# Kernel optimization log

Hardware: AMD Instinct MI355X
Metric: run time of the kernel (lower is better)

Reference implementation:

```python
import jax, jax.numpy as jnp
import numpy as np

WINDOW = 3
SEQ_LEN = 41
FEATURE = 128
FILTER_NUM = 128
PAD = WINDOW // 2


def setup_inputs() -> dict:
    key = jax.random.key(0)
    k1, k2 = jax.random.split(key)
    B = 4096
    inputs = jax.random.normal(k1, (B, SEQ_LEN, FEATURE), dtype=jnp.float32)
    # per-position Linear weights: 41 independent [window*feature -> filter_num] layers
    fan_in = WINDOW * FEATURE
    W = jax.random.normal(k2, (SEQ_LEN, fan_in, FILTER_NUM), dtype=jnp.float32) / np.sqrt(fan_in)
    b = jnp.zeros((SEQ_LEN, FILTER_NUM), dtype=jnp.float32)
    return {"inputs": inputs, "W": W, "b": b}


def reference(inputs, W, b):
    # inputs: [B, S, F]; pad sequence dim by PAD zeros on each side
    xpad = jnp.pad(inputs, ((0, 0), (PAD, PAD), (0, 0)))  # [B, S+2*PAD, F]
    # gather windows: idx[s, w] = s + w -> [B, S, WINDOW, F]
    idx = jnp.arange(SEQ_LEN)[:, None] + jnp.arange(WINDOW)[None, :]
    xw = xpad[:, idx, :]
    B = inputs.shape[0]
    xw = xw.reshape(B, SEQ_LEN, WINDOW * FEATURE)  # [B, S, W*F]
    # per-position linear (locally-connected): one batched GEMM over positions
    out = jnp.einsum('bsd,sdf->bsf', xw, W) + b[None, :, :]
    # ReLU; Dropout(0.5) is identity in eval mode
    return jax.nn.relu(out)
```

## Files before the change

kernel.cpp:

```cpp
#include <hip/hip_runtime.h>

#define SEQ 41
#define FEAT 128
#define KDIM 384
#define ROWLEN (SEQ * FEAT)
#define BM 128

typedef float floatx4 __attribute__((ext_vector_type(4)));
typedef __bf16 bf16x8 __attribute__((ext_vector_type(8)));
typedef unsigned short ushortx8 __attribute__((ext_vector_type(8)));

__device__ __forceinline__ unsigned short f2bf(float f) {
    unsigned int u = __builtin_bit_cast(unsigned int, f);
    return (unsigned short)((u + 0x7fffu + ((u >> 16) & 1u)) >> 16);
}

__device__ __forceinline__ bf16x8 pack8(floatx4 lo, floatx4 hi) {
    bf16x8 r;
#pragma unroll
    for (int j = 0; j < 4; j++) { r[j] = (__bf16)lo[j]; r[4 + j] = (__bf16)hi[j]; }
    return r;
}

__global__ __launch_bounds__(256) void wt2_kernel(const float* __restrict__ W,
                                                  unsigned short* __restrict__ Wt2) {
    int t = blockIdx.x * 256 + threadIdx.x;
    int s = t / 6144, g = t % 6144;
    int lane = g & 63, nt = (g >> 6) & 7, ks = (g >> 9) & 1, slab = g >> 10;
    int n  = nt * 16 + (lane & 15);
    int k0 = slab * 64 + ks * 32 + (lane >> 4) * 8;
    const float* Ws = W + (size_t)s * KDIM * FEAT;
    ushortx8 v;
#pragma unroll
    for (int j = 0; j < 8; j++) v[j] = f2bf(Ws[(size_t)(k0 + j) * FEAT + n]);
    *reinterpret_cast<ushortx8*>(Wt2 + (size_t)t * 8) = v;
}

template <int USE_WT>
__global__ __launch_bounds__(256, 3) void gemm_kernel(const float* __restrict__ X,
                                                      const void* __restrict__ Wsrc,
                                                      const float* __restrict__ bias,
                                                      float* __restrict__ out) {
    const int tid  = threadIdx.x;
    const int lane = tid & 63;
    const int wv   = tid >> 6;
    const int s    = blockIdx.y;
    const int m0   = blockIdx.x * BM + wv * 32;

    const int klo = (s == 0) ? 2 : 0;
    const int khi = (s == SEQ - 1) ? 4 : 6;
    const int nst = (khi - klo) * 2;

    const int colq = lane & 15, quad = lane >> 4;

    const int koff = (s - 1) * FEAT + klo * 64 + quad * 8;
    const float* aptr0 = X + (size_t)(m0 + colq) * ROWLEN + koff;
    const float* aptr1 = aptr0 + (size_t)16 * ROWLEN;

    const unsigned short* Wt2 = (const unsigned short*)Wsrc;
    const float* Wf = (const float*)Wsrc;
    const unsigned short* bptr = Wt2 + ((size_t)s * 6 + klo) * 8192 + lane * 8;

    floatx4 acc[2][8];
#pragma unroll
    for (int mi = 0; mi < 2; mi++)
#pragma unroll
        for (int ni = 0; ni < 8; ni++) acc[mi][ni] = (floatx4){0.f, 0.f, 0.f, 0.f};

    floatx4 aL0[2], aH0[2], aL1[2], aH1[2];

    auto loadA = [&](floatx4 (&L)[2], floatx4 (&H)[2], int ksi) {
        const float* p0 = aptr0 + ksi * 32;
        const float* p1 = aptr1 + ksi * 32;
        L[0] = *reinterpret_cast<const floatx4*>(p0);
        H[0] = *reinterpret_cast<const floatx4*>(p0 + 4);
        L[1] = *reinterpret_cast<const floatx4*>(p1);
        H[1] = *reinterpret_cast<const floatx4*>(p1 + 4);
    };

    auto step = [&](floatx4 (&L)[2], floatx4 (&H)[2], int ksi) {
        bf16x8 bfr[8];
        if (USE_WT) {
            const unsigned short* bp = bptr + (size_t)ksi * 4096;
#pragma unroll
            for (int ni = 0; ni < 8; ni++)
                bfr[ni] = *reinterpret_cast<const bf16x8*>(bp + ni * 512);
        } else {
            int kk = klo * 64 + ksi * 32 + quad * 8;
#pragma unroll
            for (int ni = 0; ni < 8; ni++) {
                ushortx8 v;
#pragma unroll
                for (int j = 0; j < 8; j++)
                    v[j] = f2bf(Wf[((size_t)s * KDIM + kk + j) * FEAT + ni * 16 + colq]);
                bfr[ni] = __builtin_bit_cast(bf16x8, v);
            }
        }
        bf16x8 af0 = pack8(L[0], H[0]);
        bf16x8 af1 = pack8(L[1], H[1]);
        __builtin_amdgcn_s_setprio(1);
#pragma unroll
        for (int ni = 0; ni < 8; ni++) {
            acc[0][ni] = __builtin_amdgcn_mfma_f32_16x16x32_bf16(af0, bfr[ni], acc[0][ni], 0, 0, 0);
            acc[1][ni] = __builtin_amdgcn_mfma_f32_16x16x32_bf16(af1, bfr[ni], acc[1][ni], 0, 0, 0);
        }
        __builtin_amdgcn_s_setprio(0);
    };

    loadA(aL0, aH0, 0);
    for (int ksi = 0; ksi < nst; ksi += 2) {
        loadA(aL1, aH1, ksi + 1);
        step(aL0, aH0, ksi);
        if (ksi + 2 < nst) loadA(aL0, aH0, ksi + 2);
        step(aL1, aH1, ksi + 1);
    }

#pragma unroll
    for (int ni = 0; ni < 8; ni++) {
        int n = ni * 16 + colq;
        float bv = bias[s * FEAT + n];
#pragma unroll
        for (int mi = 0; mi < 2; mi++) {
            size_t base = ((size_t)(m0 + mi * 16 + quad * 4) * SEQ + s) * FEAT + n;
#pragma unroll
            for (int r = 0; r < 4; r++) {
                float v = acc[mi][ni][r] + bv;
                v = v > 0.f ? v : 0.f;
                out[base + (size_t)r * (SEQ * FEAT)] = v;
            }
        }
    }
}

extern "C" void kernel_launch(void* const* d_in, const int* in_sizes, int n_in,
                              void* d_out, int out_size, void* d_ws, size_t ws_size,
                              hipStream_t stream) {
    const float* X    = (const float*)d_in[0];
    const float* W    = (const float*)d_in[1];
    const float* bias = (const float*)d_in[2];
    float* out = (float*)d_out;

    const int B = in_sizes[0] / ROWLEN;
    dim3 grid(B / BM, SEQ);

    const size_t wt_bytes = (size_t)SEQ * 6 * 8192 * sizeof(unsigned short);
    if (ws_size >= wt_bytes) {
        unsigned short* Wt2 = (unsigned short*)d_ws;
        wt2_kernel<<<(SEQ * 6144) / 256, 256, 0, stream>>>(W, Wt2);
        gemm_kernel<1><<<grid, 256, 0, stream>>>(X, (const void*)Wt2, bias, out);
    } else {
        gemm_kernel<0><<<grid, 256, 0, stream>>>(X, (const void*)W, bias, out);
    }
}
```

Before: 202.3 us.

## Stage per-position weights in LDS via async DMA with larger 512-thread tiles

The GEMM block grows to 256 rows and 8 waves. The whole per-position bf16 weight slab (up to 96KB) is loaded once into shared memory with global_load_lds, so waves no longer each read B fragments from global/L2. The A loads are prefetched four steps deep in registers to hide latency. In exchange there is a large LDS footprint that limits occupancy, a full-slab barrier before any compute, and more register pressure from the four A buffers.

```diff
diff --git a/kernel.cpp b/kernel.cpp
--- a/kernel.cpp
+++ b/kernel.cpp
@@ -4,7 +4,7 @@
 #define FEAT 128
 #define KDIM 384
 #define ROWLEN (SEQ * FEAT)
-#define BM 128
+#define BM 256
 
 typedef float floatx4 __attribute__((ext_vector_type(4)));
 typedef __bf16 bf16x8 __attribute__((ext_vector_type(8)));
@@ -22,6 +22,11 @@
     return r;
 }
 
+#define DMA16(g, l)                                                          \
+    __builtin_amdgcn_global_load_lds(                                        \
+        (const __attribute__((address_space(1))) void*)(g),                  \
+        (__attribute__((address_space(3))) void*)(l), 16, 0, 0)
+
 __global__ __launch_bounds__(256) void wt2_kernel(const float* __restrict__ W,
                                                   unsigned short* __restrict__ Wt2) {
     int t = blockIdx.x * 256 + threadIdx.x;
@@ -37,10 +42,12 @@
 }
 
 template <int USE_WT>
-__global__ __launch_bounds__(256, 3) void gemm_kernel(const float* __restrict__ X,
+__global__ __launch_bounds__(512, 2) void gemm_kernel(const float* __restrict__ X,
                                                       const void* __restrict__ Wsrc,
                                                       const float* __restrict__ bias,
                                                       float* __restrict__ out) {
+    __shared__ unsigned short Bs[6 * 8192];
+
     const int tid  = threadIdx.x;
     const int lane = tid & 63;
     const int wv   = tid >> 6;
@@ -49,7 +56,8 @@
 
     const int klo = (s == 0) ? 2 : 0;
     const int khi = (s == SEQ - 1) ? 4 : 6;
-    const int nst = (khi - klo) * 2;
+    const int nk  = khi - klo;
+    const int nst = nk * 2;
 
     const int colq = lane & 15, quad = lane >> 4;
 
@@ -57,47 +65,32 @@
     const float* aptr0 = X + (size_t)(m0 + colq) * ROWLEN + koff;
     const float* aptr1 = aptr0 + (size_t)16 * ROWLEN;
 
-    const unsigned short* Wt2 = (const unsigned short*)Wsrc;
-    const float* Wf = (const float*)Wsrc;
-    const unsigned short* bptr = Wt2 + ((size_t)s * 6 + klo) * 8192 + lane * 8;
-
     floatx4 acc[2][8];
 #pragma unroll
     for (int mi = 0; mi < 2; mi++)
 #pragma unroll
         for (int ni = 0; ni < 8; ni++) acc[mi][ni] = (floatx4){0.f, 0.f, 0.f, 0.f};
 
-    floatx4 aL0[2], aH0[2], aL1[2], aH1[2];
+    struct Abuf { floatx4 L0, H0, L1, H1; };
+    Abuf A0, A1, A2, A3;
 
-    auto loadA = [&](floatx4 (&L)[2], floatx4 (&H)[2], int ksi) {
+    auto loadA = [&](Abuf& ab, int ksi) {
         const float* p0 = aptr0 + ksi * 32;
         const float* p1 = aptr1 + ksi * 32;
-        L[0] = *reinterpret_cast<const floatx4*>(p0);
-        H[0] = *reinterpret_cast<const floatx4*>(p0 + 4);
-        L[1] = *reinterpret_cast<const floatx4*>(p1);
-        H[1] = *reinterpret_cast<const floatx4*>(p1 + 4);
+        ab.L0 = *reinterpret_cast<const floatx4*>(p0);
+        ab.H0 = *reinterpret_cast<const floatx4*>(p0 + 4);
+        ab.L1 = *reinterpret_cast<const floatx4*>(p1);
+        ab.H1 = *reinterpret_cast<const floatx4*>(p1 + 4);
     };
 
-    auto step = [&](floatx4 (&L)[2], floatx4 (&H)[2], int ksi) {
+    auto step = [&](const Abuf& ab, int ksi) {
         bf16x8 bfr[8];
-        if (USE_WT) {
-            const unsigned short* bp = bptr + (size_t)ksi * 4096;
+        const unsigned short* bp = &Bs[ksi * 4096 + lane * 8];
 #pragma unroll
-            for (int ni = 0; ni < 8; ni++)
-                bfr[ni] = *reinterpret_cast<const bf16x8*>(bp + ni * 512);
-        } else {
-            int kk = klo * 64 + ksi * 32 + quad * 8;
-#pragma unroll
-            for (int ni = 0; ni < 8; ni++) {
-                ushortx8 v;
-#pragma unroll
-                for (int j = 0; j < 8; j++)
-                    v[j] = f2bf(Wf[((size_t)s * KDIM + kk + j) * FEAT + ni * 16 + colq]);
-                bfr[ni] = __builtin_bit_cast(bf16x8, v);
-            }
-        }
-        bf16x8 af0 = pack8(L[0], H[0]);
-        bf16x8 af1 = pack8(L[1], H[1]);
+        for (int ni = 0; ni < 8; ni++)
+            bfr[ni] = *reinterpret_cast<const bf16x8*>(bp + ni * 512);
+        bf16x8 af0 = pack8(ab.L0, ab.H0);
+        bf16x8 af1 = pack8(ab.L1, ab.H1);
         __builtin_amdgcn_s_setprio(1);
 #pragma unroll
         for (int ni = 0; ni < 8; ni++) {
@@ -107,13 +100,37 @@
         __builtin_amdgcn_s_setprio(0);
     };
 
-    loadA(aL0, aH0, 0);
-    for (int ksi = 0; ksi < nst; ksi += 2) {
-        loadA(aL1, aH1, ksi + 1);
-        step(aL0, aH0, ksi);
-        if (ksi + 2 < nst) loadA(aL0, aH0, ksi + 2);
-        step(aL1, aH1, ksi + 1);
+    loadA(A0, 0); loadA(A1, 1); loadA(A2, 2); loadA(A3, 3);
+
+    if (USE_WT) {
+        const unsigned short* wsrc =
+            (const unsigned short*)Wsrc + ((size_t)s * 6 + klo) * 8192;
+        const int nwi = nk * 16;
+        for (int i = wv; i < nwi; i += 8)
+            DMA16(wsrc + (size_t)i * 512 + lane * 8, &Bs[(size_t)i * 512]);
+    } else {
+        const float* Wf = (const float*)Wsrc;
+        for (int j = tid; j < nk * 1024; j += 512) {
+            int ln = j & 63, nt = (j >> 6) & 7, ksa = j >> 9;
+            int k = klo * 64 + ksa * 32 + (ln >> 4) * 8;
+            int n = nt * 16 + (ln & 15);
+            ushortx8 v;
+#pragma unroll
+            for (int jj = 0; jj < 8; jj++)
+                v[jj] = f2bf(Wf[((size_t)s * KDIM + k + jj) * FEAT + n]);
+            *reinterpret_cast<ushortx8*>(&Bs[(size_t)j * 8]) = v;
+        }
     }
+    __syncthreads();
+
+    int ksi = 0;
+    for (; ksi + 4 < nst; ksi += 4) {
+        step(A0, ksi + 0); loadA(A0, ksi + 4);
+        step(A1, ksi + 1); loadA(A1, ksi + 5);
+        step(A2, ksi + 2); loadA(A2, ksi + 6);
+        step(A3, ksi + 3); loadA(A3, ksi + 7);
+    }
+    step(A0, ksi + 0); step(A1, ksi + 1); step(A2, ksi + 2); step(A3, ksi + 3);
 
 #pragma unroll
     for (int ni = 0; ni < 8; ni++) {
@@ -147,8 +164,8 @@
     if (ws_size >= wt_bytes) {
         unsigned short* Wt2 = (unsigned short*)d_ws;
         wt2_kernel<<<(SEQ * 6144) / 256, 256, 0, stream>>>(W, Wt2);
-        gemm_kernel<1><<<grid, 256, 0, stream>>>(X, (const void*)Wt2, bias, out);
+        gemm_kernel<1><<<grid, 512, 0, stream>>>(X, (const void*)Wt2, bias, out);
     } else {
-        gemm_kernel<0><<<grid, 256, 0, stream>>>(X, (const void*)W, bias, out);
+        gemm_kernel<0><<<grid, 512, 0, stream>>>(X, (const void*)W, bias, out);
     }
 }
```

Measured after the change: 192.1 us. -5.0%, faster.
